# Performance work log

Hardware: AMD Instinct MI355X
Metric: run time of the kernel (lower is better)

Reference implementation:

```python
import jax, jax.numpy as jnp
import numpy as np

N_NODES = 100000
N_EDGES = 3200000
IN_CH = 128
HID_CH = 64
NEG_SLOPE = 0.2  # PyG GATConv default leaky_relu slope


def setup_inputs() -> dict:
    key = jax.random.key(0)
    k1, k2, k3, k4, k5, k6 = jax.random.split(key, 6)
    x = jax.random.normal(k1, (N_NODES, IN_CH), dtype=jnp.float32)
    edge_index = jax.random.randint(k2, (2, N_EDGES), 0, N_NODES, dtype=jnp.int64)
    # learned params of GATConv(in, hid, heads=1)
    W = jax.random.normal(k3, (IN_CH, HID_CH), dtype=jnp.float32) / np.sqrt(IN_CH)
    att_src = jax.random.normal(k4, (HID_CH,), dtype=jnp.float32) / np.sqrt(HID_CH)
    att_dst = jax.random.normal(k5, (HID_CH,), dtype=jnp.float32) / np.sqrt(HID_CH)
    bias = jax.random.normal(k6, (HID_CH,), dtype=jnp.float32) * 0.01
    return {"x": x, "edge_index": edge_index, "W": W, "att_src": att_src,
            "att_dst": att_dst, "bias": bias}


def reference(x, edge_index, W, att_src, att_dst, bias):
    N = x.shape[0]
    h = x @ W  # [N, H] linear transform
    # PyG GATConv default: add self loops
    loops = jnp.arange(N, dtype=edge_index.dtype)
    src = jnp.concatenate([edge_index[0], loops])  # [E+N]
    dst = jnp.concatenate([edge_index[1], loops])
    # per-node attention halves, then gather per-edge
    a_src = h @ att_src  # [N]
    a_dst = h @ att_dst  # [N]
    e = jax.nn.leaky_relu(a_src[src] + a_dst[dst], NEG_SLOPE)  # [E+N]
    # segment softmax over incoming edges of each destination node
    m = jax.ops.segment_max(e, dst, num_segments=N)
    e = jnp.exp(e - m[dst])
    s = jax.ops.segment_sum(e, dst, num_segments=N)
    alpha = e / s[dst]  # [E+N]
    # scatter-aggregate weighted source features
    out = jax.ops.segment_sum(h[src] * alpha[:, None], dst, num_segments=N) + bias
    return out, alpha[:, None]
```

## Files before the change

kernel.cpp:

```cpp
#include <hip/hip_runtime.h>
#include <hip/hip_bf16.h>

#define IN_CH 128
#define HID 64
#define NEG_SLOPE 0.2f
#define BSH 8
#define CAP 10240
#define KPT 20

typedef __attribute__((ext_vector_type(8))) short short8;
typedef __attribute__((ext_vector_type(4))) float floatx4;
typedef __attribute__((ext_vector_type(2))) float f32x2;

__device__ inline short bfr(float f) {
    unsigned u = __float_as_uint(f);
    u += 0x7fffu + ((u >> 16) & 1u);
    return (short)(u >> 16);
}

__global__ void k_prep(const float* __restrict__ W, short* __restrict__ wfrag,
                       int* __restrict__ g_cursor)
{
    if (blockIdx.x == 0) {
        g_cursor[threadIdx.x] = 0;
        g_cursor[threadIdx.x + 256] = 0;
    }
    int idx = blockIdx.x * 256 + threadIdx.x;
    if (idx >= 1024) return;
    int f = idx >> 6, l = idx & 63;
    int kt = f >> 2, nt = f & 3;
    int k0 = kt * 32 + (l >> 4) * 8;
    int n = nt * 16 + (l & 15);
#pragma unroll
    for (int j = 0; j < 8; ++j)
        wfrag[idx * 8 + j] = bfr(W[(k0 + j) * HID + n]);
}

__global__ __launch_bounds__(256) void k_gemm(
    const float* __restrict__ x, const short8* __restrict__ wfrag,
    const float* __restrict__ att_src, const float* __restrict__ att_dst,
    short* __restrict__ h, float* __restrict__ a_src,
    float* __restrict__ a_dst, int N)
{
    const int t = threadIdx.x;
    const int lane = t & 63;
    const int wv = t >> 6;
    const int l15 = lane & 15;
    const int quad = lane >> 4;

    short8 bf[16];
#pragma unroll
    for (int f = 0; f < 16; ++f) bf[f] = wfrag[f * 64 + lane];

    float as4[4], ad4[4];
#pragma unroll
    for (int nt = 0; nt < 4; ++nt) {
        as4[nt] = att_src[nt * 16 + l15];
        ad4[nt] = att_dst[nt * 16 + l15];
    }

    const int rowbase = blockIdx.x * 128 + wv * 32;

#pragma unroll
    for (int mt = 0; mt < 2; ++mt) {
        const int m0 = rowbase + mt * 16;
        const int rowa = m0 + l15;
        const int rowc = rowa < N ? rowa : N - 1;
        const float* xp = x + (size_t)rowc * IN_CH + quad * 8;

        short8 af[4];
#pragma unroll
        for (int kt = 0; kt < 4; ++kt) {
            float4 p0 = *(const float4*)(xp + kt * 32);
            float4 p1 = *(const float4*)(xp + kt * 32 + 4);
            short8 a;
            a[0] = bfr(p0.x); a[1] = bfr(p0.y); a[2] = bfr(p0.z); a[3] = bfr(p0.w);
            a[4] = bfr(p1.x); a[5] = bfr(p1.y); a[6] = bfr(p1.z); a[7] = bfr(p1.w);
            af[kt] = a;
        }

        floatx4 acc[4];
#pragma unroll
        for (int nt = 0; nt < 4; ++nt) acc[nt] = (floatx4){0.f, 0.f, 0.f, 0.f};
#pragma unroll
        for (int kt = 0; kt < 4; ++kt)
#pragma unroll
            for (int nt = 0; nt < 4; ++nt)
                acc[nt] = __builtin_amdgcn_mfma_f32_16x16x32_bf16(
                    af[kt], bf[kt * 4 + nt], acc[nt], 0, 0, 0);

#pragma unroll
        for (int r = 0; r < 4; ++r) {
            const int row = m0 + quad * 4 + r;
            const bool ok = row < N;
            if (ok) {
#pragma unroll
                for (int nt = 0; nt < 4; ++nt)
                    h[(size_t)row * HID + nt * 16 + l15] = bfr(acc[nt][r]);
            }
            float ps = acc[0][r] * as4[0] + acc[1][r] * as4[1] +
                       acc[2][r] * as4[2] + acc[3][r] * as4[3];
            float pd = acc[0][r] * ad4[0] + acc[1][r] * ad4[1] +
                       acc[2][r] * ad4[2] + acc[3][r] * ad4[3];
#pragma unroll
            for (int m2 = 1; m2 < 16; m2 <<= 1) {
                ps += __shfl_xor(ps, m2, 64);
                pd += __shfl_xor(pd, m2, 64);
            }
            if (ok && l15 == 0) { a_src[row] = ps; a_dst[row] = pd; }
        }
    }
}

__global__ __launch_bounds__(256) void k_binB(
    const int* __restrict__ ei, int* __restrict__ g_cursor,
    int* __restrict__ pairs, int E, int nb)
{
    __shared__ int hist[512];
    __shared__ int base[512];
    const int t = threadIdx.x;
    hist[t] = 0;
    hist[t + 256] = 0;
    __syncthreads();

    int s[16], d[16], l[16];
    const int4* s4 = (const int4*)ei;
    const int4* d4 = (const int4*)(ei + E);
    const int E4 = E >> 2;
    const int q0 = blockIdx.x * 1024;
#pragma unroll
    for (int i = 0; i < 4; ++i) {
        int q = q0 + i * 256 + t;
        int4 sv = make_int4(0, 0, 0, 0);
        int4 dv = make_int4(-1, -1, -1, -1);
        if (q < E4) { sv = s4[q]; dv = d4[q]; }
        s[4 * i + 0] = sv.x; s[4 * i + 1] = sv.y; s[4 * i + 2] = sv.z; s[4 * i + 3] = sv.w;
        d[4 * i + 0] = dv.x; d[4 * i + 1] = dv.y; d[4 * i + 2] = dv.z; d[4 * i + 3] = dv.w;
    }
#pragma unroll
    for (int i = 0; i < 16; ++i)
        if (d[i] >= 0) l[i] = atomicAdd(&hist[d[i] >> BSH], 1);
    __syncthreads();

    if (t < nb) base[t] = atomicAdd(&g_cursor[t], hist[t]);
    if (t + 256 < nb) base[t + 256] = atomicAdd(&g_cursor[t + 256], hist[t + 256]);
    __syncthreads();

#pragma unroll
    for (int i = 0; i < 16; ++i) {
        if (d[i] < 0) continue;
        int b = d[i] >> BSH;
        int pos = base[b] + l[i];
        if (pos < CAP)
            pairs[b * CAP + pos] = s[i] | ((d[i] & 255) << 17);
    }
}

__global__ __launch_bounds__(512) void k_binC(
    const int* __restrict__ pairs, const int* __restrict__ g_cursor,
    int* __restrict__ row_start, int* __restrict__ cnt,
    int* __restrict__ csr_src, int N, int nb)
{
    __shared__ int h0[256];
    __shared__ int hs[512];
    __shared__ int exc[256];
    __shared__ int sbase;
    const int t = threadIdx.x;
    const int b = blockIdx.x;
    int m = g_cursor[b];
    if (m > CAP) m = CAP;
    const int* pb = pairs + b * CAP;

    int bv = (t < nb) ? g_cursor[t] : 0;
    hs[t] = bv;
    __syncthreads();
    for (int off = 1; off < 512; off <<= 1) {
        int u = (t >= off) ? hs[t - off] : 0;
        __syncthreads();
        hs[t] += u;
        __syncthreads();
    }
    if (t == b) sbase = hs[t] - bv;
    if (t < 256) h0[t] = 0;
    __syncthreads();

    int p[KPT], l[KPT];
#pragma unroll
    for (int k = 0; k < KPT; ++k) {
        const int i = t + k * 512;
        if (i < m) {
            p[k] = pb[i];
            l[k] = atomicAdd(&h0[p[k] >> 17], 1);
        }
    }
    __syncthreads();

    if (t < 256) hs[t] = h0[t];
    __syncthreads();
    for (int off = 1; off < 256; off <<= 1) {
        int u = (t >= off && t < 256) ? hs[t - off] : 0;
        __syncthreads();
        if (t < 256) hs[t] += u;
        __syncthreads();
    }
    const int basec = sbase;
    if (t < 256) {
        const int e0 = hs[t] - h0[t];
        exc[t] = e0;
        const int dd = (b << BSH) + t;
        if (dd < N) { row_start[dd] = basec + e0; cnt[dd] = h0[t]; }
    }
    __syncthreads();

#pragma unroll
    for (int k = 0; k < KPT; ++k) {
        const int i = t + k * 512;
        if (i < m) {
            const int dl = p[k] >> 17;
            csr_src[basec + exc[dl] + l[k]] = p[k] & 0x1FFFF;
        }
    }
}

__global__ __launch_bounds__(256) void k_agg(
    const __hip_bfloat16* __restrict__ h, const float* __restrict__ a_src,
    const float* __restrict__ a_dst, const float* __restrict__ bias,
    const int* __restrict__ row_start, const int* __restrict__ cnt,
    const int* __restrict__ csr_src,
    float* __restrict__ out, float2* __restrict__ adi, int N)
{
    __shared__ float red[4][2][576];

    const int wave = threadIdx.x >> 6;
    const int lane = threadIdx.x & 63;
    const int d0 = blockIdx.x * 8 + wave * 2;
    if (d0 >= N) return;
    const int d1 = d0 + 1;
    const bool has1 = d1 < N;

    const int q  = lane >> 3;
    const int i8 = lane & 7;

    const float2 ad2 = *(const float2*)(a_dst + d0);
    const float ad0 = ad2.x;
    const float ad1 = ad2.y;
    const int2 cn2 = *(const int2*)(cnt + d0);
    const int n0 = cn2.x;
    const int n1 = has1 ? cn2.y : 0;
    const int st0 = row_start[d0];
    const int en0 = st0 + n0;
    const int st1 = en0;
    const int en1 = st1 + n1;

    const uint4* h4 = (const uint4*)h;

    float ps0 = 0.f, ps1 = 0.f;
    f32x2 ac0[4], ac1[4];
#pragma unroll
    for (int c = 0; c < 4; ++c) {
        ac0[c] = (f32x2){0.f, 0.f};
        ac1[c] = (f32x2){0.f, 0.f};
    }

    const int nbt0 = (n0 + 63) >> 6;
    const int nbt1 = (n1 + 63) >> 6;
    const int nbm = nbt0 > nbt1 ? nbt0 : nbt1;

    int b0 = st0, b1 = st1;
    for (int it = 0; it < nbm; ++it, b0 += 64, b1 += 64) {
        int s0v = 0, s1v = 0;
        float e0 = 0.f, e1 = 0.f;
        const int idx0 = b0 + lane;
        if (it < nbt0 && idx0 < en0) {
            s0v = csr_src[idx0];
            float v = a_src[s0v] + ad0;
            v = v > 0.f ? v : NEG_SLOPE * v;
            e0 = __expf(v);
            ps0 += e0;
        }
        const int idx1 = b1 + lane;
        if (it < nbt1 && idx1 < en1) {
            s1v = csr_src[idx1];
            float v = a_src[s1v] + ad1;
            v = v > 0.f ? v : NEG_SLOPE * v;
            e1 = __expf(v);
            ps1 += e1;
        }
        const int m0 = (it < nbt0) ? min(64, en0 - b0) : 0;
        const int m1 = (it < nbt1) ? min(64, en1 - b1) : 0;
        const int mm = m0 > m1 ? m0 : m1;
#pragma unroll 4
        for (int j = 0; j < mm; j += 8) {
            const int jq = j + q;
            const int sj0 = __shfl(s0v, jq, 64);
            const float ej0 = __shfl(e0, jq, 64);
            const int sj1 = __shfl(s1v, jq, 64);
            const float ej1 = __shfl(e1, jq, 64);
            uint4 u0 = h4[(size_t)sj0 * 8 + i8];
            uint4 u1 = h4[(size_t)sj1 * 8 + i8];
            f32x2 ev0; ev0[0] = ej0; ev0[1] = ej0;
            f32x2 ev1; ev1[0] = ej1; ev1[1] = ej1;
            f32x2 c;
            c[0] = __uint_as_float(u0.x << 16);
            c[1] = __uint_as_float(u0.x & 0xffff0000u);
            ac0[0] = __builtin_elementwise_fma(ev0, c, ac0[0]);
            c[0] = __uint_as_float(u0.y << 16);
            c[1] = __uint_as_float(u0.y & 0xffff0000u);
            ac0[1] = __builtin_elementwise_fma(ev0, c, ac0[1]);
            c[0] = __uint_as_float(u0.z << 16);
            c[1] = __uint_as_float(u0.z & 0xffff0000u);
            ac0[2] = __builtin_elementwise_fma(ev0, c, ac0[2]);
            c[0] = __uint_as_float(u0.w << 16);
            c[1] = __uint_as_float(u0.w & 0xffff0000u);
            ac0[3] = __builtin_elementwise_fma(ev0, c, ac0[3]);
            c[0] = __uint_as_float(u1.x << 16);
            c[1] = __uint_as_float(u1.x & 0xffff0000u);
            ac1[0] = __builtin_elementwise_fma(ev1, c, ac1[0]);
            c[0] = __uint_as_float(u1.y << 16);
            c[1] = __uint_as_float(u1.y & 0xffff0000u);
            ac1[1] = __builtin_elementwise_fma(ev1, c, ac1[1]);
            c[0] = __uint_as_float(u1.z << 16);
            c[1] = __uint_as_float(u1.z & 0xffff0000u);
            ac1[2] = __builtin_elementwise_fma(ev1, c, ac1[2]);
            c[0] = __uint_as_float(u1.w << 16);
            c[1] = __uint_as_float(u1.w & 0xffff0000u);
            ac1[3] = __builtin_elementwise_fma(ev1, c, ac1[3]);
        }
    }

    float* r0 = &red[wave][0][0];
    float* r1 = &red[wave][1][0];
#pragma unroll
    for (int p = 0; p < 4; ++p) {
        r0[(i8 * 8 + 2 * p) * 9 + q]     = ac0[p][0];
        r0[(i8 * 8 + 2 * p + 1) * 9 + q] = ac0[p][1];
        r1[(i8 * 8 + 2 * p) * 9 + q]     = ac1[p][0];
        r1[(i8 * 8 + 2 * p + 1) * 9 + q] = ac1[p][1];
    }

#pragma unroll
    for (int m2 = 32; m2 > 0; m2 >>= 1) {
        ps0 += __shfl_xor(ps0, m2, 64);
        ps1 += __shfl_xor(ps1, m2, 64);
    }

    const float2 asd = *(const float2*)(a_src + d0);
    float vs0 = asd.x + ad0;
    vs0 = vs0 > 0.f ? vs0 : NEG_SLOPE * vs0;
    const float es0 = __expf(vs0);
    const float inv0 = 1.f / (ps0 + es0);
    float es1 = 0.f, inv1 = 0.f;
    if (has1) {
        float vs1 = asd.y + ad1;
        vs1 = vs1 > 0.f ? vs1 : NEG_SLOPE * vs1;
        es1 = __expf(vs1);
        inv1 = 1.f / (ps1 + es1);
    }
    if (lane == 0) {
        adi[d0] = make_float2(ad0, inv0);
        if (has1) adi[d1] = make_float2(ad1, inv1);
    }

    float s0 = 0.f, s1 = 0.f;
#pragma unroll
    for (int qq = 0; qq < 8; ++qq) {
        s0 += r0[lane * 9 + qq];
        s1 += r1[lane * 9 + qq];
    }

    const ushort* hu = (const ushort*)h;
    const float bi = bias[lane];
    float hs0 = __uint_as_float(((unsigned)hu[(size_t)d0 * HID + lane]) << 16);
    out[(size_t)d0 * HID + lane] = fmaf(es0, hs0, s0) * inv0 + bi;
    if (has1) {
        float hs1 = __uint_as_float(((unsigned)hu[(size_t)d1 * HID + lane]) << 16);
        out[(size_t)d1 * HID + lane] = fmaf(es1, hs1, s1) * inv1 + bi;
    }
}

__global__ void k_alpha(const int* __restrict__ ei,
                        const float* __restrict__ a_src,
                        const float2* __restrict__ adi,
                        float* __restrict__ out_alpha, int E, int N)
{
    const int E4 = E >> 2;
    const int i = blockIdx.x * 256 + threadIdx.x;
    if (i < E4) {
        const int4 sv = ((const int4*)ei)[i];
        const int4 dv = ((const int4*)(ei + E))[i];
        float4 o;
        {
            const float2 av = adi[dv.x];
            float v = a_src[sv.x] + av.x;
            v = v > 0.f ? v : NEG_SLOPE * v;
            o.x = __expf(v) * av.y;
        }
        {
            const float2 av = adi[dv.y];
            float v = a_src[sv.y] + av.x;
            v = v > 0.f ? v : NEG_SLOPE * v;
            o.y = __expf(v) * av.y;
        }
        {
            const float2 av = adi[dv.z];
            float v = a_src[sv.z] + av.x;
            v = v > 0.f ? v : NEG_SLOPE * v;
            o.z = __expf(v) * av.y;
        }
        {
            const float2 av = adi[dv.w];
            float v = a_src[sv.w] + av.x;
            v = v > 0.f ? v : NEG_SLOPE * v;
            o.w = __expf(v) * av.y;
        }
        ((float4*)out_alpha)[i] = o;
    } else {
        const int j = i - E4;
        if (j < N) {
            const float2 av = adi[j];
            float v = a_src[j] + av.x;
            v = v > 0.f ? v : NEG_SLOPE * v;
            out_alpha[E + j] = __expf(v) * av.y;
        }
    }
}

extern "C" void kernel_launch(void* const* d_in, const int* in_sizes, int n_in,
                              void* d_out, int out_size, void* d_ws, size_t ws_size,
                              hipStream_t stream)
{
    (void)n_in; (void)out_size; (void)ws_size;
    const float* x       = (const float*)d_in[0];
    const int*   ei      = (const int*)d_in[1];
    const float* W       = (const float*)d_in[2];
    const float* att_src = (const float*)d_in[3];
    const float* att_dst = (const float*)d_in[4];
    const float* bias    = (const float*)d_in[5];

    const int N = in_sizes[0] / IN_CH;
    const int E = in_sizes[1] / 2;
    const int nb = (N + 255) >> BSH;

    __hip_bfloat16* h = (__hip_bfloat16*)d_ws;
    float* a_src_d = (float*)(h + (size_t)N * HID);
    float* a_dst_d = a_src_d + N;
    float2* adi    = (float2*)(a_dst_d + N);
    int* row_start = (int*)(adi + N);
    int* cnt       = row_start + N;
    int* g_cursor  = cnt + N;
    short* wfrag   = (short*)(g_cursor + 512);
    int* pairs     = (int*)(wfrag + 8192);
    int* csr_src   = pairs + (size_t)nb * CAP;

    float* out       = (float*)d_out;
    float* out_alpha = out + (size_t)N * HID;

    k_prep<<<4, 256, 0, stream>>>(W, wfrag, g_cursor);
    k_gemm<<<(N + 127) / 128, 256, 0, stream>>>(x, (const short8*)wfrag,
                                                att_src, att_dst,
                                                (short*)h, a_src_d, a_dst_d, N);
    k_binB<<<(E / 4 + 1023) / 1024, 256, 0, stream>>>(ei, g_cursor, pairs, E, nb);
    k_binC<<<nb, 512, 0, stream>>>(pairs, g_cursor,
                                   row_start, cnt, csr_src, N, nb);
    k_agg<<<(N + 7) / 8, 256, 0, stream>>>(h, a_src_d, a_dst_d, bias,
                                           row_start, cnt, csr_src,
                                           out, adi, N);
    k_alpha<<<((E >> 2) + N + 255) / 256, 256, 0, stream>>>(ei, a_src_d, adi,
                                                            out_alpha, E, N);
}
```

Measured before the change: 272.9 us.

## Fuse weight prep into GEMM and merge binning kernels via grid sync

Removes the separate weight-prep kernel: each GEMM block now stages W into LDS and converts it to bf16 MFMA fragments itself, and block 0 clears the bin cursors. The two edge-binning kernels are merged into one cooperative kernel that uses a grid-wide sync between bucket scatter and per-bucket CSR build. The CSR phase rereads pairs and places edges with LDS atomic cursors instead of keeping them in registers. This saves kernel launches and gaps, but adds per-block W loads, extra LDS use that can lower GEMM occupancy, a grid-sync cost, and a second pass over pairs.

```diff
diff --git a/kernel.cpp b/kernel.cpp
--- a/kernel.cpp
+++ b/kernel.cpp
@@ -1,12 +1,14 @@
 #include <hip/hip_runtime.h>
 #include <hip/hip_bf16.h>
+#include <hip/hip_cooperative_groups.h>
+
+namespace cg = cooperative_groups;
 
 #define IN_CH 128
 #define HID 64
 #define NEG_SLOPE 0.2f
 #define BSH 8
 #define CAP 10240
-#define KPT 20
 
 typedef __attribute__((ext_vector_type(8))) short short8;
 typedef __attribute__((ext_vector_type(4))) float floatx4;
@@ -18,39 +20,43 @@
     return (short)(u >> 16);
 }
 
-__global__ void k_prep(const float* __restrict__ W, short* __restrict__ wfrag,
-                       int* __restrict__ g_cursor)
-{
-    if (blockIdx.x == 0) {
-        g_cursor[threadIdx.x] = 0;
-        g_cursor[threadIdx.x + 256] = 0;
-    }
-    int idx = blockIdx.x * 256 + threadIdx.x;
-    if (idx >= 1024) return;
-    int f = idx >> 6, l = idx & 63;
-    int kt = f >> 2, nt = f & 3;
-    int k0 = kt * 32 + (l >> 4) * 8;
-    int n = nt * 16 + (l & 15);
-#pragma unroll
-    for (int j = 0; j < 8; ++j)
-        wfrag[idx * 8 + j] = bfr(W[(k0 + j) * HID + n]);
-}
-
 __global__ __launch_bounds__(256) void k_gemm(
-    const float* __restrict__ x, const short8* __restrict__ wfrag,
+    const float* __restrict__ x, const float* __restrict__ W,
     const float* __restrict__ att_src, const float* __restrict__ att_dst,
     short* __restrict__ h, float* __restrict__ a_src,
-    float* __restrict__ a_dst, int N)
+    float* __restrict__ a_dst, int* __restrict__ g_cursor, int N)
 {
+    __shared__ float wlds[IN_CH * 65];
+
     const int t = threadIdx.x;
     const int lane = t & 63;
     const int wv = t >> 6;
     const int l15 = lane & 15;
     const int quad = lane >> 4;
 
+    if (blockIdx.x == 0) { g_cursor[t] = 0; g_cursor[t + 256] = 0; }
+
+#pragma unroll
+    for (int r = 0; r < 8; ++r) {
+        const int idx4 = r * 256 + t;
+        const float4 w4 = ((const float4*)W)[idx4];
+        const int fi = idx4 * 4;
+        float* dst = &wlds[(fi >> 6) * 65 + (fi & 63)];
+        dst[0] = w4.x; dst[1] = w4.y; dst[2] = w4.z; dst[3] = w4.w;
+    }
+    __syncthreads();
+
     short8 bf[16];
 #pragma unroll
-    for (int f = 0; f < 16; ++f) bf[f] = wfrag[f * 64 + lane];
+    for (int f = 0; f < 16; ++f) {
+        const int kt = f >> 2, nt = f & 3;
+        const int k0 = kt * 32 + quad * 8;
+        const int n = nt * 16 + l15;
+        short8 a;
+#pragma unroll
+        for (int j = 0; j < 8; ++j) a[j] = bfr(wlds[(k0 + j) * 65 + n]);
+        bf[f] = a;
+    }
 
     float as4[4], ad4[4];
 #pragma unroll
@@ -112,30 +118,36 @@
     }
 }
 
-__global__ __launch_bounds__(256) void k_binB(
+__global__ __launch_bounds__(512, 4) void k_sort(
     const int* __restrict__ ei, int* __restrict__ g_cursor,
-    int* __restrict__ pairs, int E, int nb)
+    int* __restrict__ pairs, int* __restrict__ row_start,
+    int* __restrict__ cnt, int* __restrict__ csr_src, int E, int N, int nb)
 {
     __shared__ int hist[512];
     __shared__ int base[512];
+    __shared__ int cur[256];
+    __shared__ int sbase;
+
     const int t = threadIdx.x;
+    const int b = blockIdx.x;
+
     hist[t] = 0;
-    hist[t + 256] = 0;
-    __syncthreads();
+    __syncthreads();
+
+    const int E4 = E >> 2;
+    const int C4 = (E4 + nb - 1) / nb;
+    const int q0 = b * C4;
+    const int q1 = min(q0 + C4, E4);
 
     int s[16], d[16], l[16];
-    const int4* s4 = (const int4*)ei;
-    const int4* d4 = (const int4*)(ei + E);
-    const int E4 = E >> 2;
-    const int q0 = blockIdx.x * 1024;
-#pragma unroll
-    for (int i = 0; i < 4; ++i) {
-        int q = q0 + i * 256 + t;
+#pragma unroll
+    for (int k = 0; k < 4; ++k) {
+        const int q = q0 + k * 512 + t;
         int4 sv = make_int4(0, 0, 0, 0);
         int4 dv = make_int4(-1, -1, -1, -1);
-        if (q < E4) { sv = s4[q]; dv = d4[q]; }
-        s[4 * i + 0] = sv.x; s[4 * i + 1] = sv.y; s[4 * i + 2] = sv.z; s[4 * i + 3] = sv.w;
-        d[4 * i + 0] = dv.x; d[4 * i + 1] = dv.y; d[4 * i + 2] = dv.z; d[4 * i + 3] = dv.w;
+        if (q < q1) { sv = ((const int4*)ei)[q]; dv = ((const int4*)(ei + E))[q]; }
+        s[4 * k + 0] = sv.x; s[4 * k + 1] = sv.y; s[4 * k + 2] = sv.z; s[4 * k + 3] = sv.w;
+        d[4 * k + 0] = dv.x; d[4 * k + 1] = dv.y; d[4 * k + 2] = dv.z; d[4 * k + 3] = dv.w;
     }
 #pragma unroll
     for (int i = 0; i < 16; ++i)
@@ -143,82 +155,61 @@
     __syncthreads();
 
     if (t < nb) base[t] = atomicAdd(&g_cursor[t], hist[t]);
-    if (t + 256 < nb) base[t + 256] = atomicAdd(&g_cursor[t + 256], hist[t + 256]);
     __syncthreads();
 
 #pragma unroll
     for (int i = 0; i < 16; ++i) {
         if (d[i] < 0) continue;
-        int b = d[i] >> BSH;
-        int pos = base[b] + l[i];
+        const int bb = d[i] >> BSH;
+        const int pos = base[bb] + l[i];
         if (pos < CAP)
-            pairs[b * CAP + pos] = s[i] | ((d[i] & 255) << 17);
-    }
-}
-
-__global__ __launch_bounds__(512) void k_binC(
-    const int* __restrict__ pairs, const int* __restrict__ g_cursor,
-    int* __restrict__ row_start, int* __restrict__ cnt,
-    int* __restrict__ csr_src, int N, int nb)
-{
-    __shared__ int h0[256];
-    __shared__ int hs[512];
-    __shared__ int exc[256];
-    __shared__ int sbase;
-    const int t = threadIdx.x;
-    const int b = blockIdx.x;
+            pairs[bb * CAP + pos] = s[i] | ((d[i] & 255) << 17);
+    }
+
+    cg::this_grid().sync();
+
     int m = g_cursor[b];
     if (m > CAP) m = CAP;
     const int* pb = pairs + b * CAP;
 
-    int bv = (t < nb) ? g_cursor[t] : 0;
-    hs[t] = bv;
+    const int bv = (t < nb) ? g_cursor[t] : 0;
+    hist[t] = bv;
     __syncthreads();
     for (int off = 1; off < 512; off <<= 1) {
-        int u = (t >= off) ? hs[t - off] : 0;
+        int u = (t >= off) ? hist[t - off] : 0;
         __syncthreads();
-        hs[t] += u;
+        hist[t] += u;
         __syncthreads();
     }
-    if (t == b) sbase = hs[t] - bv;
-    if (t < 256) h0[t] = 0;
-    __syncthreads();
-
-    int p[KPT], l[KPT];
-#pragma unroll
-    for (int k = 0; k < KPT; ++k) {
-        const int i = t + k * 512;
-        if (i < m) {
-            p[k] = pb[i];
-            l[k] = atomicAdd(&h0[p[k] >> 17], 1);
-        }
-    }
-    __syncthreads();
-
-    if (t < 256) hs[t] = h0[t];
+    if (t == b) sbase = hist[t] - bv;
+    if (t < 256) base[t] = 0;
+    __syncthreads();
+    const int basec = sbase;
+
+    for (int i = t; i < m; i += 512)
+        atomicAdd(&base[pb[i] >> 17], 1);
+    __syncthreads();
+
+    if (t < 256) hist[t] = base[t];
     __syncthreads();
     for (int off = 1; off < 256; off <<= 1) {
-        int u = (t >= off && t < 256) ? hs[t - off] : 0;
+        int u = (t >= off && t < 256) ? hist[t - off] : 0;
         __syncthreads();
-        if (t < 256) hs[t] += u;
+        if (t < 256) hist[t] += u;
         __syncthreads();
     }
-    const int basec = sbase;
     if (t < 256) {
-        const int e0 = hs[t] - h0[t];
-        exc[t] = e0;
+        const int e0 = hist[t] - base[t];
+        cur[t] = basec + e0;
         const int dd = (b << BSH) + t;
-        if (dd < N) { row_start[dd] = basec + e0; cnt[dd] = h0[t]; }
-    }
-    __syncthreads();
-
-#pragma unroll
-    for (int k = 0; k < KPT; ++k) {
-        const int i = t + k * 512;
-        if (i < m) {
-            const int dl = p[k] >> 17;
-            csr_src[basec + exc[dl] + l[k]] = p[k] & 0x1FFFF;
-        }
+        if (dd < N) { row_start[dd] = basec + e0; cnt[dd] = base[t]; }
+    }
+    __syncthreads();
+
+    for (int i = t; i < m; i += 512) {
+        const int p = pb[i];
+        const int pos = atomicAdd(&cur[p >> 17], 1);
+        csr_src[pos] = p & 0x1FFFF;
     }
 }
 
@@ -448,20 +439,22 @@
     int* row_start = (int*)(adi + N);
     int* cnt       = row_start + N;
     int* g_cursor  = cnt + N;
-    short* wfrag   = (short*)(g_cursor + 512);
-    int* pairs     = (int*)(wfrag + 8192);
+    int* pairs     = g_cursor + 512;
     int* csr_src   = pairs + (size_t)nb * CAP;
 
     float* out       = (float*)d_out;
     float* out_alpha = out + (size_t)N * HID;
 
-    k_prep<<<4, 256, 0, stream>>>(W, wfrag, g_cursor);
-    k_gemm<<<(N + 127) / 128, 256, 0, stream>>>(x, (const short8*)wfrag,
-                                                att_src, att_dst,
-                                                (short*)h, a_src_d, a_dst_d, N);
-    k_binB<<<(E / 4 + 1023) / 1024, 256, 0, stream>>>(ei, g_cursor, pairs, E, nb);
-    k_binC<<<nb, 512, 0, stream>>>(pairs, g_cursor,
-                                   row_start, cnt, csr_src, N, nb);
+    k_gemm<<<(N + 127) / 128, 256, 0, stream>>>(x, W, att_src, att_dst,
+                                                (short*)h, a_src_d, a_dst_d,
+                                                g_cursor, N);
+
+    void* sargs[] = { (void*)&ei, (void*)&g_cursor, (void*)&pairs,
+                      (void*)&row_start, (void*)&cnt, (void*)&csr_src,
+                      (void*)&E, (void*)&N, (void*)&nb };
+    hipLaunchCooperativeKernel((void*)k_sort, dim3(nb), dim3(512),
+                               sargs, 0, stream);
+
     k_agg<<<(N + 7) / 8, 256, 0, stream>>>(h, a_src_d, a_dst_d, bias,
                                            row_start, cnt, csr_src,
                                            out, adi, N);
```

Measured after the change: 341.0 us. 1.25x slower.

## Rework CSR binning scatter with per-row atomic cursors and split aggregation launch

Applied to the files above, without the earlier changes.

k_binB now runs with 512 threads per block, each handling 8 edges instead of 16. k_binC no longer keeps KPT=20 pairs per thread in registers. It makes two vectorized int4 passes over the pairs, one to build the histogram and one to scatter via atomic cursors in shared memory. This lowers register pressure and raises occupancy, at the cost of reading the pairs twice and making the order within each CSR row nondeterministic. The aggregation kernel is also split into two launches covering halves of the node range, which adds launch overhead for no clear reason.

```diff
diff --git a/kernel.cpp b/kernel.cpp
--- a/kernel.cpp
+++ b/kernel.cpp
@@ -6,7 +6,6 @@
 #define NEG_SLOPE 0.2f
 #define BSH 8
 #define CAP 10240
-#define KPT 20
 
 typedef __attribute__((ext_vector_type(8))) short short8;
 typedef __attribute__((ext_vector_type(4))) float floatx4;
@@ -112,7 +111,7 @@
     }
 }
 
-__global__ __launch_bounds__(256) void k_binB(
+__global__ __launch_bounds__(512) void k_binB(
     const int* __restrict__ ei, int* __restrict__ g_cursor,
     int* __restrict__ pairs, int E, int nb)
 {
@@ -120,17 +119,16 @@
     __shared__ int base[512];
     const int t = threadIdx.x;
     hist[t] = 0;
-    hist[t + 256] = 0;
-    __syncthreads();
-
-    int s[16], d[16], l[16];
+    __syncthreads();
+
+    int s[8], d[8], l[8];
     const int4* s4 = (const int4*)ei;
     const int4* d4 = (const int4*)(ei + E);
     const int E4 = E >> 2;
     const int q0 = blockIdx.x * 1024;
 #pragma unroll
-    for (int i = 0; i < 4; ++i) {
-        int q = q0 + i * 256 + t;
+    for (int i = 0; i < 2; ++i) {
+        int q = q0 + i * 512 + t;
         int4 sv = make_int4(0, 0, 0, 0);
         int4 dv = make_int4(-1, -1, -1, -1);
         if (q < E4) { sv = s4[q]; dv = d4[q]; }
@@ -138,16 +136,15 @@
         d[4 * i + 0] = dv.x; d[4 * i + 1] = dv.y; d[4 * i + 2] = dv.z; d[4 * i + 3] = dv.w;
     }
 #pragma unroll
-    for (int i = 0; i < 16; ++i)
+    for (int i = 0; i < 8; ++i)
         if (d[i] >= 0) l[i] = atomicAdd(&hist[d[i] >> BSH], 1);
     __syncthreads();
 
     if (t < nb) base[t] = atomicAdd(&g_cursor[t], hist[t]);
-    if (t + 256 < nb) base[t + 256] = atomicAdd(&g_cursor[t + 256], hist[t + 256]);
-    __syncthreads();
-
-#pragma unroll
-    for (int i = 0; i < 16; ++i) {
+    __syncthreads();
+
+#pragma unroll
+    for (int i = 0; i < 8; ++i) {
         if (d[i] < 0) continue;
         int b = d[i] >> BSH;
         int pos = base[b] + l[i];
@@ -163,13 +160,14 @@
 {
     __shared__ int h0[256];
     __shared__ int hs[512];
-    __shared__ int exc[256];
+    __shared__ int cur[256];
     __shared__ int sbase;
     const int t = threadIdx.x;
     const int b = blockIdx.x;
     int m = g_cursor[b];
     if (m > CAP) m = CAP;
-    const int* pb = pairs + b * CAP;
+    const int4* pb4 = (const int4*)(pairs + b * CAP);
+    const int m4 = (m + 3) >> 2;
 
     int bv = (t < nb) ? g_cursor[t] : 0;
     hs[t] = bv;
@@ -183,14 +181,20 @@
     if (t == b) sbase = hs[t] - bv;
     if (t < 256) h0[t] = 0;
     __syncthreads();
-
-    int p[KPT], l[KPT];
-#pragma unroll
-    for (int k = 0; k < KPT; ++k) {
-        const int i = t + k * 512;
-        if (i < m) {
-            p[k] = pb[i];
-            l[k] = atomicAdd(&h0[p[k] >> 17], 1);
+    const int basec = sbase;
+
+    for (int i4 = t; i4 < m4; i4 += 512) {
+        const int4 p = pb4[i4];
+        const int i = i4 << 2;
+        if (i + 3 < m) {
+            atomicAdd(&h0[p.x >> 17], 1);
+            atomicAdd(&h0[p.y >> 17], 1);
+            atomicAdd(&h0[p.z >> 17], 1);
+            atomicAdd(&h0[p.w >> 17], 1);
+        } else {
+            if (i     < m) atomicAdd(&h0[p.x >> 17], 1);
+            if (i + 1 < m) atomicAdd(&h0[p.y >> 17], 1);
+            if (i + 2 < m) atomicAdd(&h0[p.z >> 17], 1);
         }
     }
     __syncthreads();
@@ -203,21 +207,32 @@
         if (t < 256) hs[t] += u;
         __syncthreads();
     }
-    const int basec = sbase;
     if (t < 256) {
-        const int e0 = hs[t] - h0[t];
-        exc[t] = e0;
+        const int excl = hs[t] - h0[t];
+        cur[t] = basec + excl;
         const int dd = (b << BSH) + t;
-        if (dd < N) { row_start[dd] = basec + e0; cnt[dd] = h0[t]; }
-    }
-    __syncthreads();
-
-#pragma unroll
-    for (int k = 0; k < KPT; ++k) {
-        const int i = t + k * 512;
+        if (dd < N) { row_start[dd] = basec + excl; cnt[dd] = h0[t]; }
+    }
+    __syncthreads();
+
+    for (int i4 = t; i4 < m4; i4 += 512) {
+        const int4 p = pb4[i4];
+        const int i = i4 << 2;
         if (i < m) {
-            const int dl = p[k] >> 17;
-            csr_src[basec + exc[dl] + l[k]] = p[k] & 0x1FFFF;
+            int pos = atomicAdd(&cur[p.x >> 17], 1);
+            csr_src[pos] = p.x & 0x1FFFF;
+        }
+        if (i + 1 < m) {
+            int pos = atomicAdd(&cur[p.y >> 17], 1);
+            csr_src[pos] = p.y & 0x1FFFF;
+        }
+        if (i + 2 < m) {
+            int pos = atomicAdd(&cur[p.z >> 17], 1);
+            csr_src[pos] = p.z & 0x1FFFF;
+        }
+        if (i + 3 < m) {
+            int pos = atomicAdd(&cur[p.w >> 17], 1);
+            csr_src[pos] = p.w & 0x1FFFF;
         }
     }
 }
@@ -227,13 +242,13 @@
     const float* __restrict__ a_dst, const float* __restrict__ bias,
     const int* __restrict__ row_start, const int* __restrict__ cnt,
     const int* __restrict__ csr_src,
-    float* __restrict__ out, float2* __restrict__ adi, int N)
+    float* __restrict__ out, float2* __restrict__ adi, int dbase, int N)
 {
     __shared__ float red[4][2][576];
 
     const int wave = threadIdx.x >> 6;
     const int lane = threadIdx.x & 63;
-    const int d0 = blockIdx.x * 8 + wave * 2;
+    const int d0 = dbase + blockIdx.x * 8 + wave * 2;
     if (d0 >= N) return;
     const int d1 = d0 + 1;
     const bool has1 = d1 < N;
@@ -459,12 +474,17 @@
     k_gemm<<<(N + 127) / 128, 256, 0, stream>>>(x, (const short8*)wfrag,
                                                 att_src, att_dst,
                                                 (short*)h, a_src_d, a_dst_d, N);
-    k_binB<<<(E / 4 + 1023) / 1024, 256, 0, stream>>>(ei, g_cursor, pairs, E, nb);
+    k_binB<<<(E / 4 + 1023) / 1024, 512, 0, stream>>>(ei, g_cursor, pairs, E, nb);
     k_binC<<<nb, 512, 0, stream>>>(pairs, g_cursor,
                                    row_start, cnt, csr_src, N, nb);
-    k_agg<<<(N + 7) / 8, 256, 0, stream>>>(h, a_src_d, a_dst_d, bias,
+
+    const int H = 50000;
+    k_agg<<<(H + 7) / 8, 256, 0, stream>>>(h, a_src_d, a_dst_d, bias,
                                            row_start, cnt, csr_src,
-                                           out, adi, N);
+                                           out, adi, 0, H);
+    k_agg<<<(N - H + 7) / 8, 256, 0, stream>>>(h, a_src_d, a_dst_d, bias,
+                                               row_start, cnt, csr_src,
+                                               out, adi, H, N);
     k_alpha<<<((E >> 2) + N + 255) / 256, 256, 0, stream>>>(ei, a_src_d, adi,
                                                             out_alpha, E, N);
 }
```

Result: no change. 275.9 us (+1.1%).
